# Performance work log

Hardware: AMD Instinct MI355X
Metric: run time of the kernel (lower is better)

The kernel has to match this reference:

```python
import jax, jax.numpy as jnp
import numpy as np

N = 50000      # number of nodes
E = 800000     # number of edges (avg degree 16)
DIN = 128
DOUT = 128
EPS = 1e-06


def setup_inputs() -> dict:
    key = jax.random.key(0)
    ks = jax.random.split(key, 10)
    scale = 1.0 / np.sqrt(DIN)
    return {
        "mean": jax.random.normal(ks[0], (N, DIN), dtype=jnp.float32),
        "var": jax.random.uniform(ks[1], (N, DIN), dtype=jnp.float32),
        "W_mean": jax.random.normal(ks[2], (DIN, DOUT), dtype=jnp.float32) * scale,
        "b_mean": jax.random.normal(ks[3], (DOUT,), dtype=jnp.float32) * scale,
        "W_var": jax.random.normal(ks[4], (DIN, DOUT), dtype=jnp.float32) * scale,
        "b_var": jax.random.normal(ks[5], (DOUT,), dtype=jnp.float32) * scale,
        "adj0_w": jax.random.uniform(ks[6], (E,), dtype=jnp.float32),
        "adj1_w": jax.random.uniform(ks[7], (E,), dtype=jnp.float32),
        "edge_src": jax.random.randint(ks[8], (E,), 0, N, dtype=jnp.int32),
        "edge_dst": jax.random.randint(ks[9], (E,), 0, N, dtype=jnp.int32),
    }


def reference(mean, var, W_mean, b_mean, W_var, b_var, adj0_w, adj1_w, edge_src, edge_dst):
    # Dense projections (dropout is identity in eval mode)
    m = jax.nn.elu(mean @ W_mean + b_mean)            # [N, DOUT]
    v = jax.nn.relu(var @ W_var + b_var) + EPS        # [N, DOUT]
    # Elementwise attention gate
    att = jnp.exp(-v)
    m = m * att
    v = v * att * att
    # SpMM aggregation: out[dst] += w * x[src]  (COO edge list)
    n = mean.shape[0]
    out_m = jax.ops.segment_sum(adj0_w[:, None] * m[edge_src], edge_dst, num_segments=n)
    out_v = jax.ops.segment_sum(adj1_w[:, None] * v[edge_src], edge_dst, num_segments=n)
    return out_m, out_v
```

## Files before the change

kernel.cpp:

```cpp
#include <hip/hip_runtime.h>
#include <hip/hip_bf16.h>
#include <math.h>

#define N_NODES 50000
#define DIN     128
#define DOUT    128
#define EPS_    1e-6f
#define N_WAVES 3125
#define NBKT    196
#define EPB     2048
#define EPT     8
#define SLOT_CAP 4992
#define NB_PROJ 782

typedef __attribute__((ext_vector_type(8))) short  bf16x8;
typedef __attribute__((ext_vector_type(4))) float  f32x4;
typedef unsigned short ushort_t;

__device__ __forceinline__ ushort_t f2bf(float f) {
    unsigned u = __float_as_uint(f);
    return (ushort_t)((u + 0x7fffu + ((u >> 16) & 1u)) >> 16);
}
__device__ __forceinline__ float bflo(unsigned u) { return __uint_as_float(u << 16); }
__device__ __forceinline__ float bfhi(unsigned u) { return __uint_as_float(u & 0xffff0000u); }

__global__ __launch_bounds__(256) void prep_w_kernel(
    const float* __restrict__ Wm, const float* __restrict__ Wv,
    ushort_t* __restrict__ fm, ushort_t* __restrict__ fv,
    int* __restrict__ gcur, int* __restrict__ gh)
{
    const int gid = blockIdx.x * 256 + threadIdx.x;
    if (gid < N_NODES) gh[gid] = 0;
    if (gid < NBKT)    gcur[gid] = 0;
    if (gid < DIN * DOUT) {
        const int k = gid >> 7, n = gid & 127;
        const int ct = n >> 4, kk = k >> 5, quad = (k >> 3) & 3, j = k & 7;
        const int idx = ((ct * 4 + kk) * 64 + quad * 16 + (n & 15)) * 8 + j;
        fm[idx] = f2bf(Wm[gid]);
        fv[idx] = f2bf(Wv[gid]);
    }
}

__global__ __launch_bounds__(256) void fused_projA_kernel(
    const float* __restrict__ mean, const float* __restrict__ var,
    const float* __restrict__ bm,   const float* __restrict__ bv,
    const ushort_t* __restrict__ wfm, const ushort_t* __restrict__ wfv,
    ushort_t* __restrict__ mv,
    const int* __restrict__ src, const int* __restrict__ dst,
    const float* __restrict__ w0, const float* __restrict__ w1,
    int* __restrict__ gcur, int* __restrict__ gh,
    uint2* __restrict__ slots, int E, int nA)
{
    if ((int)blockIdx.x < nA) {
        __shared__ uint2 s_rec[EPB];
        __shared__ int   s_hist[256];
        __shared__ int   s_scn[256];
        __shared__ int   s_cur[256];
        __shared__ int   s_base[256];

        const int t  = threadIdx.x;
        const int e0 = blockIdx.x * EPB;
        const int n  = min(EPB, E - e0);

        s_hist[t] = 0;
        __syncthreads();

        int   myb[EPT];
        uint2 myr[EPT];
#pragma unroll
        for (int j = 0; j < EPT; ++j) {
            const int e = e0 + t + j * 256;
            if (e < E) {
                const int d   = dst[e];
                const int bkt = d >> 8;
                myb[j] = bkt;
                myr[j].x = (unsigned)src[e] | ((unsigned)(d & 255) << 16)
                         | ((unsigned)bkt << 24);
                myr[j].y = (unsigned)f2bf(w0[e]) | ((unsigned)f2bf(w1[e]) << 16);
                atomicAdd(&s_hist[bkt], 1);
                atomicAdd(&gh[d], 1);
            } else myb[j] = -1;
        }
        __syncthreads();

        if (t < NBKT) {
            const int c = s_hist[t];
            s_base[t] = t * SLOT_CAP + (c ? atomicAdd(&gcur[t], c) : 0);
        }
        const int x = s_hist[t];
        s_scn[t] = x;
        __syncthreads();
        for (int off = 1; off < 256; off <<= 1) {
            const int v = (t >= off) ? s_scn[t - off] : 0;
            __syncthreads();
            s_scn[t] += v;
            __syncthreads();
        }
        const int excl = s_scn[t] - x;
        __syncthreads();
        s_scn[t] = excl;
        s_cur[t] = 0;
        __syncthreads();

#pragma unroll
        for (int j = 0; j < EPT; ++j) {
            if (myb[j] >= 0) {
                const int r = atomicAdd(&s_cur[myb[j]], 1);
                s_rec[s_scn[myb[j]] + r] = myr[j];
            }
        }
        __syncthreads();

        for (int i = t; i < n; i += 256) {
            const uint2 r = s_rec[i];
            const int bkt = r.x >> 24;
            slots[s_base[bkt] + (i - s_scn[bkt])] = r;
        }
        return;
    }

    const int wave = ((int)blockIdx.x - nA) * 4 + (threadIdx.x >> 6);
    if (wave >= N_WAVES) return;
    const int lane = threadIdx.x & 63;
    const int row0 = wave * 16;
    const int kq   = lane >> 4;
    const int arow = row0 + (lane & 15);

    f32x4 accm[8], accv[8];
#pragma unroll
    for (int ct = 0; ct < 8; ++ct) {
        accm[ct] = (f32x4){0.f, 0.f, 0.f, 0.f};
        accv[ct] = (f32x4){0.f, 0.f, 0.f, 0.f};
    }

    const float* mrow = mean + (size_t)arow * DIN;
    const float* vrow = var  + (size_t)arow * DIN;

#pragma unroll
    for (int kk = 0; kk < 4; ++kk) {
        const int kb = kk * 32 + kq * 8;
        const float4 am0 = *(const float4*)(mrow + kb);
        const float4 am1 = *(const float4*)(mrow + kb + 4);
        const float4 av0 = *(const float4*)(vrow + kb);
        const float4 av1 = *(const float4*)(vrow + kb + 4);
        bf16x8 a_m, a_v;
        a_m[0]=f2bf(am0.x); a_m[1]=f2bf(am0.y); a_m[2]=f2bf(am0.z); a_m[3]=f2bf(am0.w);
        a_m[4]=f2bf(am1.x); a_m[5]=f2bf(am1.y); a_m[6]=f2bf(am1.z); a_m[7]=f2bf(am1.w);
        a_v[0]=f2bf(av0.x); a_v[1]=f2bf(av0.y); a_v[2]=f2bf(av0.z); a_v[3]=f2bf(av0.w);
        a_v[4]=f2bf(av1.x); a_v[5]=f2bf(av1.y); a_v[6]=f2bf(av1.z); a_v[7]=f2bf(av1.w);

#pragma unroll
        for (int ct = 0; ct < 8; ++ct) {
            const bf16x8 b_m = *(const bf16x8*)(wfm + ((size_t)(ct * 4 + kk) * 64 + lane) * 8);
            const bf16x8 b_v = *(const bf16x8*)(wfv + ((size_t)(ct * 4 + kk) * 64 + lane) * 8);
            accm[ct] = __builtin_amdgcn_mfma_f32_16x16x32_bf16(a_m, b_m, accm[ct], 0, 0, 0);
            accv[ct] = __builtin_amdgcn_mfma_f32_16x16x32_bf16(a_v, b_v, accv[ct], 0, 0, 0);
        }
    }

    const int par = lane & 1;
#pragma unroll
    for (int ct = 0; ct < 8; ++ct) {
        const int col = ct * 16 + (lane & 15);
        const float bmc = bm[col];
        const float bvc = bv[col];
        const int dw = ct * 16 + ((lane & 15) >> 1) * 2 + par;
#pragma unroll
        for (int r = 0; r < 4; ++r) {
            const int row = row0 + kq * 4 + r;
            float m = accm[ct][r] + bmc;
            m = (m > 0.0f) ? m : (expf(m) - 1.0f);
            float v = accv[ct][r] + bvc;
            v = ((v > 0.0f) ? v : 0.0f) + EPS_;
            const float att = expf(-v);
            const unsigned um = f2bf(m * att);
            const unsigned uv = f2bf(v * att * att);
            const unsigned om = (unsigned)__shfl_xor((int)um, 1);
            const unsigned ov = (unsigned)__shfl_xor((int)uv, 1);
            const unsigned w = par ? (ov | (uv << 16)) : (um | (om << 16));
            ((unsigned*)(mv + (size_t)row * 256))[dw] = w;
        }
    }
}

__global__ __launch_bounds__(256) void place_kernel(
    const int* __restrict__ gh, const int* __restrict__ gcur,
    const uint2* __restrict__ slots, uint2* __restrict__ final_e,
    int* __restrict__ node_start)
{
    __shared__ int s_red[256];
    __shared__ int s_scn[256];
    __shared__ int s_cur[256];

    const int b = blockIdx.x;
    const int t = threadIdx.x;

    s_red[t] = (t < b) ? gcur[t] : 0;
    const int gidx = b * 256 + t;
    const int x = (gidx < N_NODES) ? gh[gidx] : 0;
    s_scn[t] = x;
    __syncthreads();

    for (int off = 128; off > 0; off >>= 1) {
        if (t < off) s_red[t] += s_red[t + off];
        __syncthreads();
    }
    const int base = s_red[0];

    for (int off = 1; off < 256; off <<= 1) {
        const int v = (t >= off) ? s_scn[t - off] : 0;
        __syncthreads();
        s_scn[t] += v;
        __syncthreads();
    }
    const int ns = base + s_scn[t] - x;
    if (gidx <= N_NODES) node_start[gidx] = ns;
    s_cur[t] = ns;
    __syncthreads();

    const int cnt = gcur[b];
    const uint2* slot = slots + (size_t)b * SLOT_CAP;
    for (int i = t; i < cnt; i += 256) {
        const uint2 r = slot[i];
        const int f = (r.x >> 16) & 255;
        const int p = atomicAdd(&s_cur[f], 1);
        final_e[p] = r;
    }
}

#define PAIR_FMA(RW, G) do {                                                 \
    const float a0 = bflo(RW), a1 = bfhi(RW);                                \
    am0 = fmaf(a0, bflo((G).x), am0); am1 = fmaf(a0, bfhi((G).x), am1);      \
    av0 = fmaf(a1, bflo((G).y), av0); av1 = fmaf(a1, bfhi((G).y), av1);      \
    am2 = fmaf(a0, bflo((G).z), am2); am3 = fmaf(a0, bfhi((G).z), am3);      \
    av2 = fmaf(a1, bflo((G).w), av2); av3 = fmaf(a1, bfhi((G).w), av3);      \
} while (0)

__global__ __launch_bounds__(256) void agg_kernel(
    const ushort_t* __restrict__ mv,
    const uint2* __restrict__ edges, const int* __restrict__ node_start,
    float* __restrict__ out_m, float* __restrict__ out_v)
{
    const int node = blockIdx.x * 4 + (threadIdx.x >> 6);
    const int lane = threadIdx.x & 63;
    const int half = lane >> 5;
    const int l    = lane & 31;
    if (node >= N_NODES) return;

    const int j0 = node_start[node];
    const int j1 = node_start[node + 1];

    float am0=0.f, am1=0.f, am2=0.f, am3=0.f;
    float av0=0.f, av1=0.f, av2=0.f, av3=0.f;

    int j = j0;

    if ((j & 1) && j < j1) {
        const uint2 r = edges[j];
        const unsigned rw = half ? 0u : r.y;
        const uint4 g = *(const uint4*)(mv + (size_t)(r.x & 0xffffu) * 256 + l * 8);
        PAIR_FMA(rw, g);
        ++j;
    }

    for (; j + 8 <= j1; j += 8) {
        const uint4 e0 = *(const uint4*)(edges + j + 0);
        const uint4 e1 = *(const uint4*)(edges + j + 2);
        const uint4 e2 = *(const uint4*)(edges + j + 4);
        const uint4 e3 = *(const uint4*)(edges + j + 6);
        const unsigned s0 = half ? e0.z : e0.x, w0 = half ? e0.w : e0.y;
        const unsigned s1 = half ? e1.z : e1.x, w1 = half ? e1.w : e1.y;
        const unsigned s2 = half ? e2.z : e2.x, w2 = half ? e2.w : e2.y;
        const unsigned s3 = half ? e3.z : e3.x, w3 = half ? e3.w : e3.y;
        const uint4 g0 = *(const uint4*)(mv + (size_t)(s0 & 0xffffu) * 256 + l * 8);
        const uint4 g1 = *(const uint4*)(mv + (size_t)(s1 & 0xffffu) * 256 + l * 8);
        const uint4 g2 = *(const uint4*)(mv + (size_t)(s2 & 0xffffu) * 256 + l * 8);
        const uint4 g3 = *(const uint4*)(mv + (size_t)(s3 & 0xffffu) * 256 + l * 8);
        PAIR_FMA(w0, g0);
        PAIR_FMA(w1, g1);
        PAIR_FMA(w2, g2);
        PAIR_FMA(w3, g3);
    }

    for (; j + 2 <= j1; j += 2) {
        const uint4 e = *(const uint4*)(edges + j);
        const unsigned s = half ? e.z : e.x, w = half ? e.w : e.y;
        const uint4 g = *(const uint4*)(mv + (size_t)(s & 0xffffu) * 256 + l * 8);
        PAIR_FMA(w, g);
    }

    if (j < j1) {
        const uint2 r = edges[j];
        const unsigned rw = half ? 0u : r.y;
        const uint4 g = *(const uint4*)(mv + (size_t)(r.x & 0xffffu) * 256 + l * 8);
        PAIR_FMA(rw, g);
    }

    am0 += __shfl_xor(am0, 32); am1 += __shfl_xor(am1, 32);
    am2 += __shfl_xor(am2, 32); am3 += __shfl_xor(am3, 32);
    av0 += __shfl_xor(av0, 32); av1 += __shfl_xor(av1, 32);
    av2 += __shfl_xor(av2, 32); av3 += __shfl_xor(av3, 32);

    if (half == 0) {
        *(float4*)(out_m + (size_t)node * DOUT + l * 4) = make_float4(am0, am1, am2, am3);
        *(float4*)(out_v + (size_t)node * DOUT + l * 4) = make_float4(av0, av1, av2, av3);
    }
}

extern "C" void kernel_launch(void* const* d_in, const int* in_sizes, int n_in,
                              void* d_out, int out_size, void* d_ws, size_t ws_size,
                              hipStream_t stream) {
    const float* mean = (const float*)d_in[0];
    const float* var  = (const float*)d_in[1];
    const float* Wm   = (const float*)d_in[2];
    const float* bm   = (const float*)d_in[3];
    const float* Wv   = (const float*)d_in[4];
    const float* bv   = (const float*)d_in[5];
    const float* a0   = (const float*)d_in[6];
    const float* a1   = (const float*)d_in[7];
    const int*   es   = (const int*)d_in[8];
    const int*   ed   = (const int*)d_in[9];
    const int    E    = in_sizes[6];

    char* ws = (char*)d_ws;
    ushort_t* mv        = (ushort_t*)ws;
    uint2* slots        = (uint2*)(ws + 25600000);
    uint2* final_e      = (uint2*)(ws + 33427456);
    int*   node_start   = (int*)  (ws + 39827456);
    int*   gh           = (int*)  (ws + 40027472);
    int*   gcur         = (int*)  (ws + 40227472);
    ushort_t* wfm       = (ushort_t*)(ws + 40228288);
    ushort_t* wfv       = wfm + 16384;

    float* out_m = (float*)d_out;
    float* out_v = out_m + (size_t)N_NODES * DOUT;

    prep_w_kernel<<<(N_NODES + 255) / 256, 256, 0, stream>>>(Wm, Wv, wfm, wfv, gcur, gh);

    const int nA = (E + EPB - 1) / EPB;
    fused_projA_kernel<<<nA + NB_PROJ, 256, 0, stream>>>(
        mean, var, bm, bv, wfm, wfv, mv,
        es, ed, a0, a1, gcur, gh, slots, E, nA);

    place_kernel<<<NBKT, 256, 0, stream>>>(
        gh, gcur, slots, final_e, node_start);

    agg_kernel<<<(N_NODES + 3) / 4, 256, 0, stream>>>(
        mv, final_e, node_start, out_m, out_v);
}
```

Baseline: 245.9 us.

## Move per-node histogram into place kernel shared memory, drop global atomics

Removes the global per-node degree histogram (800K global atomics) from the bucketing pass and instead computes per-node counts inside the place kernel from records staged in LDS, using 1024-thread blocks. Edges per bucketing block double (EPB 4096, EPT 16) and the slot capacity per bucket grows, while the prep kernel shrinks to just the weight reformat and the bucket counter reset. The change trades global atomic traffic for larger LDS use in place_kernel, which may lower occupancy, and raises per-thread register use in the bucketing pass.

After: 207.0 us. 1.19x faster.

```diff
diff --git a/kernel.cpp b/kernel.cpp
--- a/kernel.cpp
+++ b/kernel.cpp
@@ -8,9 +8,9 @@
 #define EPS_    1e-6f
 #define N_WAVES 3125
 #define NBKT    196
-#define EPB     2048
-#define EPT     8
-#define SLOT_CAP 4992
+#define EPB     4096
+#define EPT     16
+#define SLOT_CAP 5120
 #define NB_PROJ 782
 
 typedef __attribute__((ext_vector_type(8))) short  bf16x8;
@@ -27,18 +27,15 @@
 __global__ __launch_bounds__(256) void prep_w_kernel(
     const float* __restrict__ Wm, const float* __restrict__ Wv,
     ushort_t* __restrict__ fm, ushort_t* __restrict__ fv,
-    int* __restrict__ gcur, int* __restrict__ gh)
+    int* __restrict__ gcur)
 {
     const int gid = blockIdx.x * 256 + threadIdx.x;
-    if (gid < N_NODES) gh[gid] = 0;
-    if (gid < NBKT)    gcur[gid] = 0;
-    if (gid < DIN * DOUT) {
-        const int k = gid >> 7, n = gid & 127;
-        const int ct = n >> 4, kk = k >> 5, quad = (k >> 3) & 3, j = k & 7;
-        const int idx = ((ct * 4 + kk) * 64 + quad * 16 + (n & 15)) * 8 + j;
-        fm[idx] = f2bf(Wm[gid]);
-        fv[idx] = f2bf(Wv[gid]);
-    }
+    if (gid < NBKT) gcur[gid] = 0;
+    const int k = gid >> 7, n = gid & 127;
+    const int ct = n >> 4, kk = k >> 5, quad = (k >> 3) & 3, j = k & 7;
+    const int idx = ((ct * 4 + kk) * 64 + quad * 16 + (n & 15)) * 8 + j;
+    fm[idx] = f2bf(Wm[gid]);
+    fv[idx] = f2bf(Wv[gid]);
 }
 
 __global__ __launch_bounds__(256) void fused_projA_kernel(
@@ -48,8 +45,7 @@
     ushort_t* __restrict__ mv,
     const int* __restrict__ src, const int* __restrict__ dst,
     const float* __restrict__ w0, const float* __restrict__ w1,
-    int* __restrict__ gcur, int* __restrict__ gh,
-    uint2* __restrict__ slots, int E, int nA)
+    int* __restrict__ gcur, uint2* __restrict__ slots, int E, int nA)
 {
     if ((int)blockIdx.x < nA) {
         __shared__ uint2 s_rec[EPB];
@@ -78,7 +74,6 @@
                          | ((unsigned)bkt << 24);
                 myr[j].y = (unsigned)f2bf(w0[e]) | ((unsigned)f2bf(w1[e]) << 16);
                 atomicAdd(&s_hist[bkt], 1);
-                atomicAdd(&gh[d], 1);
             } else myb[j] = -1;
         }
         __syncthreads();
@@ -183,45 +178,74 @@
     }
 }
 
-__global__ __launch_bounds__(256) void place_kernel(
-    const int* __restrict__ gh, const int* __restrict__ gcur,
+__global__ __launch_bounds__(1024) void place_kernel(
+    const int* __restrict__ gcur,
     const uint2* __restrict__ slots, uint2* __restrict__ final_e,
     int* __restrict__ node_start)
 {
-    __shared__ int s_red[256];
+    __shared__ uint2 s_rec[SLOT_CAP];
+    __shared__ int s_hist[256];
     __shared__ int s_scn[256];
     __shared__ int s_cur[256];
+    __shared__ int s_red[256];
 
     const int b = blockIdx.x;
     const int t = threadIdx.x;
 
-    s_red[t] = (t < b) ? gcur[t] : 0;
-    const int gidx = b * 256 + t;
-    const int x = (gidx < N_NODES) ? gh[gidx] : 0;
-    s_scn[t] = x;
-    __syncthreads();
-
-    for (int off = 128; off > 0; off >>= 1) {
-        if (t < off) s_red[t] += s_red[t + off];
-        __syncthreads();
-    }
-    const int base = s_red[0];
-
-    for (int off = 1; off < 256; off <<= 1) {
-        const int v = (t >= off) ? s_scn[t - off] : 0;
-        __syncthreads();
-        s_scn[t] += v;
-        __syncthreads();
-    }
-    const int ns = base + s_scn[t] - x;
-    if (gidx <= N_NODES) node_start[gidx] = ns;
-    s_cur[t] = ns;
+    if (t < 256) {
+        s_red[t]  = (t < b) ? gcur[t] : 0;
+        s_hist[t] = 0;
+    }
     __syncthreads();
 
     const int cnt = gcur[b];
     const uint2* slot = slots + (size_t)b * SLOT_CAP;
-    for (int i = t; i < cnt; i += 256) {
+
+    for (int i = t; i < cnt; i += 1024) {
         const uint2 r = slot[i];
+        s_rec[i] = r;
+        atomicAdd(&s_hist[(r.x >> 16) & 255], 1);
+    }
+
+    __syncthreads();
+    if (t < 128) s_red[t] += s_red[t + 128];
+    __syncthreads();
+    if (t < 64)  s_red[t] += s_red[t + 64];
+    __syncthreads();
+    if (t < 32)  s_red[t] += s_red[t + 32];
+    __syncthreads();
+    if (t < 16)  s_red[t] += s_red[t + 16];
+    __syncthreads();
+    if (t < 8)   s_red[t] += s_red[t + 8];
+    __syncthreads();
+    if (t < 4)   s_red[t] += s_red[t + 4];
+    __syncthreads();
+    if (t < 2)   s_red[t] += s_red[t + 2];
+    __syncthreads();
+    if (t < 1)   s_red[t] += s_red[t + 1];
+    __syncthreads();
+    const int base = s_red[0];
+
+    const int x = (t < 256) ? s_hist[t] : 0;
+    if (t < 256) s_scn[t] = x;
+    __syncthreads();
+    for (int off = 1; off < 256; off <<= 1) {
+        int v = 0;
+        if (t < 256 && t >= off) v = s_scn[t - off];
+        __syncthreads();
+        if (t < 256) s_scn[t] += v;
+        __syncthreads();
+    }
+    if (t < 256) {
+        const int ns = base + s_scn[t] - x;
+        const int gidx = b * 256 + t;
+        if (gidx <= N_NODES) node_start[gidx] = ns;
+        s_cur[t] = ns;
+    }
+    __syncthreads();
+
+    for (int i = t; i < cnt; i += 1024) {
+        const uint2 r = s_rec[i];
         const int f = (r.x >> 16) & 255;
         const int p = atomicAdd(&s_cur[f], 1);
         final_e[p] = r;
@@ -325,25 +349,24 @@
     char* ws = (char*)d_ws;
     ushort_t* mv        = (ushort_t*)ws;
     uint2* slots        = (uint2*)(ws + 25600000);
-    uint2* final_e      = (uint2*)(ws + 33427456);
-    int*   node_start   = (int*)  (ws + 39827456);
-    int*   gh           = (int*)  (ws + 40027472);
-    int*   gcur         = (int*)  (ws + 40227472);
-    ushort_t* wfm       = (ushort_t*)(ws + 40228288);
+    uint2* final_e      = (uint2*)(ws + 33628160);
+    int*   node_start   = (int*)  (ws + 40028160);
+    int*   gcur         = (int*)  (ws + 40228176);
+    ushort_t* wfm       = (ushort_t*)(ws + 40228976);
     ushort_t* wfv       = wfm + 16384;
 
     float* out_m = (float*)d_out;
     float* out_v = out_m + (size_t)N_NODES * DOUT;
 
-    prep_w_kernel<<<(N_NODES + 255) / 256, 256, 0, stream>>>(Wm, Wv, wfm, wfv, gcur, gh);
+    prep_w_kernel<<<64, 256, 0, stream>>>(Wm, Wv, wfm, wfv, gcur);
 
     const int nA = (E + EPB - 1) / EPB;
     fused_projA_kernel<<<nA + NB_PROJ, 256, 0, stream>>>(
         mean, var, bm, bv, wfm, wfv, mv,
-        es, ed, a0, a1, gcur, gh, slots, E, nA);
-
-    place_kernel<<<NBKT, 256, 0, stream>>>(
-        gh, gcur, slots, final_e, node_start);
+        es, ed, a0, a1, gcur, slots, E, nA);
+
+    place_kernel<<<NBKT, 1024, 0, stream>>>(
+        gcur, slots, final_e, node_start);
 
     agg_kernel<<<(N_NODES + 3) / 4, 256, 0, stream>>>(
         mv, final_e, node_start, out_m, out_v);
```

## Merge weight prep, projection, bucketing and placement into one persistent kernel

Applied to the files above, without the earlier changes.

Replaces three launches (weight prep, fused projection/bucketing, placement) with one persistent kernel of 640 blocks. The blocks sync through atomic-counter grid barriers and claim work roles dynamically from an atomic queue. The global per-node histogram atomics are removed; the placement stage now builds per-node counts locally from each bucket's slot records and caches up to 4096 of them in LDS. Bucketing blocks now take 4096 edges each. This saves launch gaps and global atomics, but depends on all 640 blocks being co-resident for the spin barrier and adds barrier latency.

Result: slower. 453.3 us (+84.3%).

```diff
diff --git a/kernel.cpp b/kernel.cpp
--- a/kernel.cpp
+++ b/kernel.cpp
@@ -8,10 +8,11 @@
 #define EPS_    1e-6f
 #define N_WAVES 3125
 #define NBKT    196
-#define EPB     2048
-#define EPT     8
-#define SLOT_CAP 4992
+#define EPB     4096
+#define EPT     16
+#define SLOT_CAP 5120
 #define NB_PROJ 782
+#define GRID    640
 
 typedef __attribute__((ext_vector_type(8))) short  bf16x8;
 typedef __attribute__((ext_vector_type(4))) float  f32x4;
@@ -24,69 +25,202 @@
 __device__ __forceinline__ float bflo(unsigned u) { return __uint_as_float(u << 16); }
 __device__ __forceinline__ float bfhi(unsigned u) { return __uint_as_float(u & 0xffff0000u); }
 
-__global__ __launch_bounds__(256) void prep_w_kernel(
-    const float* __restrict__ Wm, const float* __restrict__ Wv,
-    ushort_t* __restrict__ fm, ushort_t* __restrict__ fv,
-    int* __restrict__ gcur, int* __restrict__ gh)
-{
-    const int gid = blockIdx.x * 256 + threadIdx.x;
-    if (gid < N_NODES) gh[gid] = 0;
-    if (gid < NBKT)    gcur[gid] = 0;
-    if (gid < DIN * DOUT) {
-        const int k = gid >> 7, n = gid & 127;
-        const int ct = n >> 4, kk = k >> 5, quad = (k >> 3) & 3, j = k & 7;
-        const int idx = ((ct * 4 + kk) * 64 + quad * 16 + (n & 15)) * 8 + j;
-        fm[idx] = f2bf(Wm[gid]);
-        fv[idx] = f2bf(Wv[gid]);
-    }
-}
-
-__global__ __launch_bounds__(256) void fused_projA_kernel(
+__device__ __forceinline__ void gbar(int* ctr) {
+    __syncthreads();
+    if (threadIdx.x == 0) {
+        __threadfence();
+        atomicAdd(ctr, 1);
+        while (atomicAdd(ctr, 0) < GRID) __builtin_amdgcn_s_sleep(4);
+        __threadfence();
+    }
+    __syncthreads();
+}
+
+__global__ __launch_bounds__(256, 3) void mega_kernel(
     const float* __restrict__ mean, const float* __restrict__ var,
-    const float* __restrict__ bm,   const float* __restrict__ bv,
-    const ushort_t* __restrict__ wfm, const ushort_t* __restrict__ wfv,
-    ushort_t* __restrict__ mv,
+    const float* __restrict__ Wm,   const float* __restrict__ bm,
+    const float* __restrict__ Wv,   const float* __restrict__ bv,
     const int* __restrict__ src, const int* __restrict__ dst,
     const float* __restrict__ w0, const float* __restrict__ w1,
-    int* __restrict__ gcur, int* __restrict__ gh,
-    uint2* __restrict__ slots, int E, int nA)
+    ushort_t* __restrict__ mv, ushort_t* __restrict__ wfm, ushort_t* __restrict__ wfv,
+    int* __restrict__ gcur, uint2* __restrict__ slots,
+    uint2* __restrict__ final_e, int* __restrict__ node_start,
+    int* __restrict__ bar, int E, int nA)
 {
-    if ((int)blockIdx.x < nA) {
-        __shared__ uint2 s_rec[EPB];
-        __shared__ int   s_hist[256];
-        __shared__ int   s_scn[256];
-        __shared__ int   s_cur[256];
-        __shared__ int   s_base[256];
-
-        const int t  = threadIdx.x;
-        const int e0 = blockIdx.x * EPB;
-        const int n  = min(EPB, E - e0);
-
+    __shared__ uint2 s_rec[EPB];
+    __shared__ int   s_hist[256], s_scn[256], s_cur[256], s_base[256];
+    __shared__ int   s_role;
+
+    const int t = threadIdx.x;
+    const int b = blockIdx.x;
+
+    {
+        const int gid = b * 256 + t;
+        if (gid < DIN * DOUT) {
+            const int k = gid >> 7, n = gid & 127;
+            const int ct = n >> 4, kk = k >> 5, quad = (k >> 3) & 3, j = k & 7;
+            const int idx = ((ct * 4 + kk) * 64 + quad * 16 + (n & 15)) * 8 + j;
+            wfm[idx] = f2bf(Wm[gid]);
+            wfv[idx] = f2bf(Wv[gid]);
+        }
+        if (b == 64 && t < NBKT) gcur[t] = 0;
+    }
+    gbar(&bar[0]);
+
+    const int nRoles = nA + NB_PROJ;
+    for (;;) {
+        __syncthreads();
+        if (t == 0) s_role = atomicAdd(&bar[2], 1);
+        __syncthreads();
+        const int role = s_role;
+        if (role >= nRoles) break;
+
+        if (role < nA) {
+            const int e0 = role * EPB;
+            const int n  = min(EPB, E - e0);
+
+            s_hist[t] = 0;
+            __syncthreads();
+
+            int   myb[EPT];
+            uint2 myr[EPT];
+#pragma unroll
+            for (int j = 0; j < EPT; ++j) {
+                const int e = e0 + t + j * 256;
+                if (e < E) {
+                    const int d   = dst[e];
+                    const int bkt = d >> 8;
+                    myb[j] = bkt;
+                    myr[j].x = (unsigned)src[e] | ((unsigned)(d & 255) << 16)
+                             | ((unsigned)bkt << 24);
+                    myr[j].y = (unsigned)f2bf(w0[e]) | ((unsigned)f2bf(w1[e]) << 16);
+                    atomicAdd(&s_hist[bkt], 1);
+                } else myb[j] = -1;
+            }
+            __syncthreads();
+
+            if (t < NBKT) {
+                const int c = s_hist[t];
+                s_base[t] = t * SLOT_CAP + (c ? atomicAdd(&gcur[t], c) : 0);
+            }
+            const int x = s_hist[t];
+            s_scn[t] = x;
+            __syncthreads();
+            for (int off = 1; off < 256; off <<= 1) {
+                const int v = (t >= off) ? s_scn[t - off] : 0;
+                __syncthreads();
+                s_scn[t] += v;
+                __syncthreads();
+            }
+            const int excl = s_scn[t] - x;
+            __syncthreads();
+            s_scn[t] = excl;
+            s_cur[t] = 0;
+            __syncthreads();
+
+#pragma unroll
+            for (int j = 0; j < EPT; ++j) {
+                if (myb[j] >= 0) {
+                    const int r = atomicAdd(&s_cur[myb[j]], 1);
+                    s_rec[s_scn[myb[j]] + r] = myr[j];
+                }
+            }
+            __syncthreads();
+
+            for (int i = t; i < n; i += 256) {
+                const uint2 r = s_rec[i];
+                const int bkt = r.x >> 24;
+                slots[s_base[bkt] + (i - s_scn[bkt])] = r;
+            }
+        } else {
+            const int wave = (role - nA) * 4 + (t >> 6);
+            if (wave < N_WAVES) {
+                const int lane = t & 63;
+                const int row0 = wave * 16;
+                const int kq   = lane >> 4;
+                const int arow = row0 + (lane & 15);
+
+                f32x4 accm[8], accv[8];
+#pragma unroll
+                for (int ct = 0; ct < 8; ++ct) {
+                    accm[ct] = (f32x4){0.f, 0.f, 0.f, 0.f};
+                    accv[ct] = (f32x4){0.f, 0.f, 0.f, 0.f};
+                }
+
+                const float* mrow = mean + (size_t)arow * DIN;
+                const float* vrow = var  + (size_t)arow * DIN;
+
+#pragma unroll
+                for (int kk = 0; kk < 4; ++kk) {
+                    const int kb = kk * 32 + kq * 8;
+                    const float4 am0 = *(const float4*)(mrow + kb);
+                    const float4 am1 = *(const float4*)(mrow + kb + 4);
+                    const float4 av0 = *(const float4*)(vrow + kb);
+                    const float4 av1 = *(const float4*)(vrow + kb + 4);
+                    bf16x8 a_m, a_v;
+                    a_m[0]=f2bf(am0.x); a_m[1]=f2bf(am0.y); a_m[2]=f2bf(am0.z); a_m[3]=f2bf(am0.w);
+                    a_m[4]=f2bf(am1.x); a_m[5]=f2bf(am1.y); a_m[6]=f2bf(am1.z); a_m[7]=f2bf(am1.w);
+                    a_v[0]=f2bf(av0.x); a_v[1]=f2bf(av0.y); a_v[2]=f2bf(av0.z); a_v[3]=f2bf(av0.w);
+                    a_v[4]=f2bf(av1.x); a_v[5]=f2bf(av1.y); a_v[6]=f2bf(av1.z); a_v[7]=f2bf(av1.w);
+
+#pragma unroll
+                    for (int ct = 0; ct < 8; ++ct) {
+                        const bf16x8 b_m = *(const bf16x8*)(wfm + ((size_t)(ct * 4 + kk) * 64 + lane) * 8);
+                        const bf16x8 b_v = *(const bf16x8*)(wfv + ((size_t)(ct * 4 + kk) * 64 + lane) * 8);
+                        accm[ct] = __builtin_amdgcn_mfma_f32_16x16x32_bf16(a_m, b_m, accm[ct], 0, 0, 0);
+                        accv[ct] = __builtin_amdgcn_mfma_f32_16x16x32_bf16(a_v, b_v, accv[ct], 0, 0, 0);
+                    }
+                }
+
+                const int par = lane & 1;
+#pragma unroll
+                for (int ct = 0; ct < 8; ++ct) {
+                    const int col = ct * 16 + (lane & 15);
+                    const float bmc = bm[col];
+                    const float bvc = bv[col];
+                    const int dw = ct * 16 + ((lane & 15) >> 1) * 2 + par;
+#pragma unroll
+                    for (int r = 0; r < 4; ++r) {
+                        const int row = row0 + kq * 4 + r;
+                        float m = accm[ct][r] + bmc;
+                        m = (m > 0.0f) ? m : (expf(m) - 1.0f);
+                        float v = accv[ct][r] + bvc;
+                        v = ((v > 0.0f) ? v : 0.0f) + EPS_;
+                        const float att = expf(-v);
+                        const unsigned um = f2bf(m * att);
+                        const unsigned uv = f2bf(v * att * att);
+                        const unsigned om = (unsigned)__shfl_xor((int)um, 1);
+                        const unsigned ov = (unsigned)__shfl_xor((int)uv, 1);
+                        const unsigned w = par ? (ov | (uv << 16)) : (um | (om << 16));
+                        ((unsigned*)(mv + (size_t)row * 256))[dw] = w;
+                    }
+                }
+            }
+        }
+    }
+    gbar(&bar[1]);
+
+    if (b < NBKT) {
+        s_base[t] = (t < b) ? gcur[t] : 0;
         s_hist[t] = 0;
         __syncthreads();
 
-        int   myb[EPT];
-        uint2 myr[EPT];
-#pragma unroll
-        for (int j = 0; j < EPT; ++j) {
-            const int e = e0 + t + j * 256;
-            if (e < E) {
-                const int d   = dst[e];
-                const int bkt = d >> 8;
-                myb[j] = bkt;
-                myr[j].x = (unsigned)src[e] | ((unsigned)(d & 255) << 16)
-                         | ((unsigned)bkt << 24);
-                myr[j].y = (unsigned)f2bf(w0[e]) | ((unsigned)f2bf(w1[e]) << 16);
-                atomicAdd(&s_hist[bkt], 1);
-                atomicAdd(&gh[d], 1);
-            } else myb[j] = -1;
-        }
-        __syncthreads();
-
-        if (t < NBKT) {
-            const int c = s_hist[t];
-            s_base[t] = t * SLOT_CAP + (c ? atomicAdd(&gcur[t], c) : 0);
-        }
+        const int cnt = gcur[b];
+        const uint2* slot = slots + (size_t)b * SLOT_CAP;
+
+        for (int i = t; i < cnt; i += 256) {
+            const uint2 r = slot[i];
+            if (i < EPB) s_rec[i] = r;
+            atomicAdd(&s_hist[(r.x >> 16) & 255], 1);
+        }
+        __syncthreads();
+
+        for (int off = 128; off > 0; off >>= 1) {
+            if (t < off) s_base[t] += s_base[t + off];
+            __syncthreads();
+        }
+        const int base = s_base[0];
+
         const int x = s_hist[t];
         s_scn[t] = x;
         __syncthreads();
@@ -96,135 +230,18 @@
             s_scn[t] += v;
             __syncthreads();
         }
-        const int excl = s_scn[t] - x;
-        __syncthreads();
-        s_scn[t] = excl;
-        s_cur[t] = 0;
-        __syncthreads();
-
-#pragma unroll
-        for (int j = 0; j < EPT; ++j) {
-            if (myb[j] >= 0) {
-                const int r = atomicAdd(&s_cur[myb[j]], 1);
-                s_rec[s_scn[myb[j]] + r] = myr[j];
-            }
-        }
-        __syncthreads();
-
-        for (int i = t; i < n; i += 256) {
-            const uint2 r = s_rec[i];
-            const int bkt = r.x >> 24;
-            slots[s_base[bkt] + (i - s_scn[bkt])] = r;
-        }
-        return;
-    }
-
-    const int wave = ((int)blockIdx.x - nA) * 4 + (threadIdx.x >> 6);
-    if (wave >= N_WAVES) return;
-    const int lane = threadIdx.x & 63;
-    const int row0 = wave * 16;
-    const int kq   = lane >> 4;
-    const int arow = row0 + (lane & 15);
-
-    f32x4 accm[8], accv[8];
-#pragma unroll
-    for (int ct = 0; ct < 8; ++ct) {
-        accm[ct] = (f32x4){0.f, 0.f, 0.f, 0.f};
-        accv[ct] = (f32x4){0.f, 0.f, 0.f, 0.f};
-    }
-
-    const float* mrow = mean + (size_t)arow * DIN;
-    const float* vrow = var  + (size_t)arow * DIN;
-
-#pragma unroll
-    for (int kk = 0; kk < 4; ++kk) {
-        const int kb = kk * 32 + kq * 8;
-        const float4 am0 = *(const float4*)(mrow + kb);
-        const float4 am1 = *(const float4*)(mrow + kb + 4);
-        const float4 av0 = *(const float4*)(vrow + kb);
-        const float4 av1 = *(const float4*)(vrow + kb + 4);
-        bf16x8 a_m, a_v;
-        a_m[0]=f2bf(am0.x); a_m[1]=f2bf(am0.y); a_m[2]=f2bf(am0.z); a_m[3]=f2bf(am0.w);
-        a_m[4]=f2bf(am1.x); a_m[5]=f2bf(am1.y); a_m[6]=f2bf(am1.z); a_m[7]=f2bf(am1.w);
-        a_v[0]=f2bf(av0.x); a_v[1]=f2bf(av0.y); a_v[2]=f2bf(av0.z); a_v[3]=f2bf(av0.w);
-        a_v[4]=f2bf(av1.x); a_v[5]=f2bf(av1.y); a_v[6]=f2bf(av1.z); a_v[7]=f2bf(av1.w);
-
-#pragma unroll
-        for (int ct = 0; ct < 8; ++ct) {
-            const bf16x8 b_m = *(const bf16x8*)(wfm + ((size_t)(ct * 4 + kk) * 64 + lane) * 8);
-            const bf16x8 b_v = *(const bf16x8*)(wfv + ((size_t)(ct * 4 + kk) * 64 + lane) * 8);
-            accm[ct] = __builtin_amdgcn_mfma_f32_16x16x32_bf16(a_m, b_m, accm[ct], 0, 0, 0);
-            accv[ct] = __builtin_amdgcn_mfma_f32_16x16x32_bf16(a_v, b_v, accv[ct], 0, 0, 0);
-        }
-    }
-
-    const int par = lane & 1;
-#pragma unroll
-    for (int ct = 0; ct < 8; ++ct) {
-        const int col = ct * 16 + (lane & 15);
-        const float bmc = bm[col];
-        const float bvc = bv[col];
-        const int dw = ct * 16 + ((lane & 15) >> 1) * 2 + par;
-#pragma unroll
-        for (int r = 0; r < 4; ++r) {
-            const int row = row0 + kq * 4 + r;
-            float m = accm[ct][r] + bmc;
-            m = (m > 0.0f) ? m : (expf(m) - 1.0f);
-            float v = accv[ct][r] + bvc;
-            v = ((v > 0.0f) ? v : 0.0f) + EPS_;
-            const float att = expf(-v);
-            const unsigned um = f2bf(m * att);
-            const unsigned uv = f2bf(v * att * att);
-            const unsigned om = (unsigned)__shfl_xor((int)um, 1);
-            const unsigned ov = (unsigned)__shfl_xor((int)uv, 1);
-            const unsigned w = par ? (ov | (uv << 16)) : (um | (om << 16));
-            ((unsigned*)(mv + (size_t)row * 256))[dw] = w;
-        }
-    }
-}
-
-__global__ __launch_bounds__(256) void place_kernel(
-    const int* __restrict__ gh, const int* __restrict__ gcur,
-    const uint2* __restrict__ slots, uint2* __restrict__ final_e,
-    int* __restrict__ node_start)
-{
-    __shared__ int s_red[256];
-    __shared__ int s_scn[256];
-    __shared__ int s_cur[256];
-
-    const int b = blockIdx.x;
-    const int t = threadIdx.x;
-
-    s_red[t] = (t < b) ? gcur[t] : 0;
-    const int gidx = b * 256 + t;
-    const int x = (gidx < N_NODES) ? gh[gidx] : 0;
-    s_scn[t] = x;
-    __syncthreads();
-
-    for (int off = 128; off > 0; off >>= 1) {
-        if (t < off) s_red[t] += s_red[t + off];
-        __syncthreads();
-    }
-    const int base = s_red[0];
-
-    for (int off = 1; off < 256; off <<= 1) {
-        const int v = (t >= off) ? s_scn[t - off] : 0;
-        __syncthreads();
-        s_scn[t] += v;
-        __syncthreads();
-    }
-    const int ns = base + s_scn[t] - x;
-    if (gidx <= N_NODES) node_start[gidx] = ns;
-    s_cur[t] = ns;
-    __syncthreads();
-
-    const int cnt = gcur[b];
-    const uint2* slot = slots + (size_t)b * SLOT_CAP;
-    for (int i = t; i < cnt; i += 256) {
-        const uint2 r = slot[i];
-        const int f = (r.x >> 16) & 255;
-        const int p = atomicAdd(&s_cur[f], 1);
-        final_e[p] = r;
+        const int ns = base + s_scn[t] - x;
+        const int gidx = b * 256 + t;
+        if (gidx <= N_NODES) node_start[gidx] = ns;
+        s_cur[t] = ns;
+        __syncthreads();
+
+        for (int i = t; i < cnt; i += 256) {
+            const uint2 r = (i < EPB) ? s_rec[i] : slot[i];
+            const int f = (r.x >> 16) & 255;
+            const int p = atomicAdd(&s_cur[f], 1);
+            final_e[p] = r;
+        }
     }
 }
 
@@ -325,25 +342,26 @@
     char* ws = (char*)d_ws;
     ushort_t* mv        = (ushort_t*)ws;
     uint2* slots        = (uint2*)(ws + 25600000);
-    uint2* final_e      = (uint2*)(ws + 33427456);
-    int*   node_start   = (int*)  (ws + 39827456);
-    int*   gh           = (int*)  (ws + 40027472);
-    int*   gcur         = (int*)  (ws + 40227472);
-    ushort_t* wfm       = (ushort_t*)(ws + 40228288);
+    uint2* final_e      = (uint2*)(ws + 33628160);
+    int*   node_start   = (int*)  (ws + 40028160);
+    int*   gcur         = (int*)  (ws + 40228176);
+    int*   bar          = (int*)  (ws + 40228960);
+    ushort_t* wfm       = (ushort_t*)(ws + 40228976);
     ushort_t* wfv       = wfm + 16384;
 
     float* out_m = (float*)d_out;
     float* out_v = out_m + (size_t)N_NODES * DOUT;
 
-    prep_w_kernel<<<(N_NODES + 255) / 256, 256, 0, stream>>>(Wm, Wv, wfm, wfv, gcur, gh);
-
     const int nA = (E + EPB - 1) / EPB;
-    fused_projA_kernel<<<nA + NB_PROJ, 256, 0, stream>>>(
-        mean, var, bm, bv, wfm, wfv, mv,
-        es, ed, a0, a1, gcur, gh, slots, E, nA);
-
-    place_kernel<<<NBKT, 256, 0, stream>>>(
-        gh, gcur, slots, final_e, node_start);
+
+    hipMemsetAsync(bar, 0, 16, stream);
+
+    mega_kernel<<<GRID, 256, 0, stream>>>(
+        mean, var, Wm, bm, Wv, bv,
+        es, ed, a0, a1,
+        mv, wfm, wfv,
+        gcur, slots, final_e, node_start,
+        bar, E, nA);
 
     agg_kernel<<<(N_NODES + 3) / 4, 256, 0, stream>>>(
         mv, final_e, node_start, out_m, out_v);
```
